# Kernel tuning notes

Hardware: AMD Instinct MI355X
Metric: run time of the kernel (lower is better)

The kernel has to match this reference:

```python
import jax, jax.numpy as jnp
import numpy as np

B, IN, OUT = 8192, 4096, 4096


def setup_inputs() -> dict:
    key = jax.random.key(0)
    k_x, k_qw, k_qb, k_pw, k_pb, k_eps, k_ps = jax.random.split(key, 7)
    x = jax.random.normal(k_x, (B, IN), jnp.float32)
    # Posterior / prior means: weight (OUT, IN) and bias (OUT,), fused as (OUT, IN+1)
    q_w = 0.05 * jax.random.normal(k_qw, (OUT, IN), jnp.float32)
    q_b = 0.05 * jax.random.normal(k_qb, (OUT,), jnp.float32)
    p_w = 0.05 * jax.random.normal(k_pw, (OUT, IN), jnp.float32)
    p_b = 0.05 * jax.random.normal(k_pb, (OUT,), jnp.float32)
    q_mu = jnp.concatenate([q_w, q_b[:, None]], axis=1)  # (OUT, IN+1)
    p_mu = jnp.concatenate([p_w, p_b[:, None]], axis=1)  # (OUT, IN+1)
    # Matches torch init: cat(0.5*log|w|, 0.5*log|b|) == 0.5*log|cat(w, b)|
    q_log_sigma = 0.5 * jnp.log(jnp.abs(q_mu))
    # Explicit reparameterization noise (torch.randn_like made deterministic)
    eps = jax.random.normal(k_eps, (OUT, IN + 1), jnp.float32)
    p_log_sigma = jnp.asarray(-2.0, jnp.float32)  # scalar prior log-std
    return {"x": x, "p_log_sigma": p_log_sigma, "q_mu": q_mu,
            "q_log_sigma": q_log_sigma, "p_mu": p_mu, "eps": eps}


def reference(x, p_log_sigma, q_mu, q_log_sigma, p_mu, eps):
    # Append ones column to absorb the bias (torch.cat([x, ones], dim=1))
    x_aug = jnp.concatenate([x, jnp.ones((x.shape[0], 1), x.dtype)], axis=1)  # (B, IN+1)
    q_sigma = jnp.exp(q_log_sigma)
    p_sigma = jnp.exp(p_log_sigma)
    # Reparameterized weight sample
    weights = q_mu + q_sigma * eps  # (OUT, IN+1)
    # KL(N(p_mu, p_sigma) || N(q_mu, q_sigma)) summed elementwise (diag branch)
    kl = jnp.sum(p_log_sigma - q_log_sigma
                 + (q_sigma ** 2 + (p_mu - q_mu) ** 2) / (2.0 * p_sigma ** 2)
                 - 0.5)
    # F.linear(x_aug, weights, zeros(OUT))
    outputs = x_aug @ weights.T  # (B, OUT)
    return outputs, kl
```

## Files before the change

### kernel.cpp

```cpp
#include <hip/hip_runtime.h>
#include <cstdint>
#include <cstddef>

#define K_PAD 4128
#define BKg 32
#define NT 129

typedef __bf16 bf16x8 __attribute__((ext_vector_type(8)));
typedef float f32x4 __attribute__((ext_vector_type(4)));

__device__ __forceinline__ unsigned short f2bf(float f) {
  unsigned int u = __float_as_uint(f);
  u = (u + 0x7fffu + ((u >> 16) & 1u)) >> 16;
  return (unsigned short)u;
}

__device__ __forceinline__ void gload_lds16(const void* g, void* l) {
  __builtin_amdgcn_global_load_lds((const __attribute__((address_space(1))) void*)g,
                                   (__attribute__((address_space(3))) void*)l,
                                   16, 0, 0);
}

__global__ void k_xaug(const float* __restrict__ x, unsigned short* __restrict__ xa) {
  const int row = blockIdx.x;
  const int t = threadIdx.x;
  const float4* xr = (const float4*)(x + (size_t)row * 4096);
  unsigned short* out = xa + (size_t)row * K_PAD;
#pragma unroll
  for (int i = 0; i < 4; ++i) {
    const int g = t + i * 256;
    float4 v = xr[g];
    ushort4 o;
    o.x = f2bf(v.x); o.y = f2bf(v.y); o.z = f2bf(v.z); o.w = f2bf(v.w);
    *(ushort4*)(out + g * 4) = o;
  }
  if (t < 32) out[4096 + t] = (t == 0) ? (unsigned short)0x3F80 : (unsigned short)0;
}

__global__ void k_wkl(const float* __restrict__ q_mu, const float* __restrict__ q_ls,
                      const float* __restrict__ p_mu, const float* __restrict__ eps,
                      const float* __restrict__ p_ls, unsigned short* __restrict__ w,
                      float* __restrict__ kl_out) {
  const int row = blockIdx.x;
  const int t = threadIdx.x;
  const float pls = p_ls[0];
  const float inv2ps2 = 0.5f * __expf(-2.0f * pls);
  const size_t base = (size_t)row * 4097;
  unsigned short* wr = w + (size_t)row * K_PAD;
  float kl = 0.f;
  const float4* qm4 = (const float4*)(q_mu + base);
  const float4* ql4 = (const float4*)(q_ls + base);
  const float4* pm4 = (const float4*)(p_mu + base);
  const float4* ep4 = (const float4*)(eps + base);
  if ((((size_t)row * 4097) & 3) == 0) {
#pragma unroll 1
    for (int i = 0; i < 4; ++i) {
      const int g = t + i * 256;
      float4 qm = qm4[g], ql = ql4[g], pm = pm4[g], ep = ep4[g];
      float kls = 0.f;
      ushort4 o;
      {
        float qs = __expf(ql.x); float d = pm.x - qm.x;
        kls += (pls - ql.x) - 0.5f + (qs * qs + d * d) * inv2ps2;
        o.x = f2bf(__fmaf_rn(qs, ep.x, qm.x));
      }
      {
        float qs = __expf(ql.y); float d = pm.y - qm.y;
        kls += (pls - ql.y) - 0.5f + (qs * qs + d * d) * inv2ps2;
        o.y = f2bf(__fmaf_rn(qs, ep.y, qm.y));
      }
      {
        float qs = __expf(ql.z); float d = pm.z - qm.z;
        kls += (pls - ql.z) - 0.5f + (qs * qs + d * d) * inv2ps2;
        o.z = f2bf(__fmaf_rn(qs, ep.z, qm.z));
      }
      {
        float qs = __expf(ql.w); float d = pm.w - qm.w;
        kls += (pls - ql.w) - 0.5f + (qs * qs + d * d) * inv2ps2;
        o.w = f2bf(__fmaf_rn(qs, ep.w, qm.w));
      }
      kl += kls;
      *(ushort4*)(wr + g * 4) = o;
    }
    if (t == 0) {
      const int c = 4096;
      float qm = q_mu[base + c], ql = q_ls[base + c];
      float qs = __expf(ql);
      float d = p_mu[base + c] - qm;
      kl += (pls - ql) - 0.5f + (qs * qs + d * d) * inv2ps2;
      wr[c] = f2bf(__fmaf_rn(qs, eps[base + c], qm));
    }
    if (t < 31) wr[4097 + t] = 0;
  } else {
#pragma unroll 1
    for (int i = 0; i < 17; ++i) {
      const int c = t + i * 256;
      if (c < 4097) {
        float qm = q_mu[base + c];
        float ql = q_ls[base + c];
        float qs = __expf(ql);
        float e  = eps[base + c];
        float pm = p_mu[base + c];
        float d = pm - qm;
        kl += (pls - ql) - 0.5f + (qs * qs + d * d) * inv2ps2;
        wr[c] = f2bf(__fmaf_rn(qs, e, qm));
      } else if (c < K_PAD) {
        wr[c] = 0;
      }
    }
  }
#pragma unroll
  for (int off = 32; off > 0; off >>= 1) kl += __shfl_down(kl, off, 64);
  __shared__ float part[4];
  const int wave = t >> 6, lane = t & 63;
  if (lane == 0) part[wave] = kl;
  __syncthreads();
  if (t == 0) atomicAdd(kl_out, part[0] + part[1] + part[2] + part[3]);
}

__global__ __launch_bounds__(512, 2) void k_gemm(const unsigned short* __restrict__ A,
                                                 const unsigned short* __restrict__ Bm,
                                                 float* __restrict__ C) {
  __shared__ unsigned short As[3][256 * 32];
  __shared__ unsigned short Bs[3][256 * 32];
  const int t = threadIdx.x;
  const int wave = t >> 6;
  const int lane = t & 63;
  const int wm = wave >> 2;
  const int wn = wave & 3;
  const int rowBase = blockIdx.y * 256;
  const int colBase = blockIdx.x * 256;
  const int fr = lane & 15;
  const int kg = lane >> 4;

  f32x4 acc[8][4] = {};

  const unsigned short* Abase = A + (size_t)rowBase * K_PAD;
  const unsigned short* Bbase = Bm + (size_t)colBase * K_PAD;

  const int rs = t >> 2;
  const int kc = ((t & 3) ^ ((t >> 3) & 3)) * 8;
  const int lds0 = (wave * 64) * 8;
  const int lds1 = (512 + wave * 64) * 8;

  int aOff[8], bOff[4];
#pragma unroll
  for (int i = 0; i < 8; ++i) {
    const int ra = wm * 128 + i * 16 + fr;
    aOff[i] = (ra * 4 + (kg ^ ((ra >> 1) & 3))) * 8;
  }
#pragma unroll
  for (int j = 0; j < 4; ++j) {
    const int rbr = wn * 64 + j * 16 + fr;
    bOff[j] = (rbr * 4 + (kg ^ ((rbr >> 1) & 3))) * 8;
  }

#define STAGE(SB, K0)                                                              \
  do {                                                                             \
    gload_lds16(Abase + (size_t)rs * K_PAD + (K0) + kc, &As[SB][lds0]);            \
    gload_lds16(Abase + (size_t)(rs + 128) * K_PAD + (K0) + kc, &As[SB][lds1]);    \
    gload_lds16(Bbase + (size_t)rs * K_PAD + (K0) + kc, &Bs[SB][lds0]);            \
    gload_lds16(Bbase + (size_t)(rs + 128) * K_PAD + (K0) + kc, &Bs[SB][lds1]);    \
  } while (0)

  STAGE(0, 0);
  STAGE(1, BKg);
  asm volatile("s_waitcnt vmcnt(4)" ::: "memory");
  __builtin_amdgcn_s_barrier();
  asm volatile("" ::: "memory");

#define BODY(RB, SB, KT)                                                           \
  do {                                                                             \
    int kn = (KT) + 2; if (kn > NT - 1) kn = NT - 1;    \
    STAGE(SB, kn * BKg);                                                           \
    bf16x8 af[4], bfv[4];                                                          \
    _Pragma("unroll") for (int j = 0; j < 4; ++j)                                  \
      bfv[j] = *(const bf16x8*)&Bs[RB][bOff[j]];                                   \
    _Pragma("unroll") for (int i = 0; i < 4; ++i)                                  \
      af[i] = *(const bf16x8*)&As[RB][aOff[i]];                                    \
    __builtin_amdgcn_s_setprio(1);                                                 \
    _Pragma("unroll") for (int i = 0; i < 4; ++i)                                  \
      _Pragma("unroll") for (int j = 0; j < 4; ++j)                                \
        acc[i][j] = __builtin_amdgcn_mfma_f32_16x16x32_bf16(af[i], bfv[j],         \
                                                            acc[i][j], 0, 0, 0);  \
    __builtin_amdgcn_s_setprio(0);                                                 \
    _Pragma("unroll") for (int i = 0; i < 4; ++i)                                  \
      af[i] = *(const bf16x8*)&As[RB][aOff[4 + i]];                                \
    __builtin_amdgcn_s_setprio(1);                                                 \
    _Pragma("unroll") for (int i = 0; i < 4; ++i)                                  \
      _Pragma("unroll") for (int j = 0; j < 4; ++j)                                \
        acc[4 + i][j] = __builtin_amdgcn_mfma_f32_16x16x32_bf16(af[i], bfv[j],     \
                                                                acc[4 + i][j],    \
                                                                0, 0, 0);          \
    __builtin_amdgcn_s_setprio(0);                                                 \
    asm volatile("s_waitcnt vmcnt(4)" ::: "memory");       \
    __builtin_amdgcn_s_barrier();                                                  \
    asm volatile("" ::: "memory");                                                 \
  } while (0)

#pragma unroll 1
  for (int kt = 0; kt < NT; kt += 3) {
    BODY(0, 2, kt);
    BODY(1, 0, kt + 1);
    BODY(2, 1, kt + 2);
  }

#undef BODY
#undef STAGE

  const int cr = (lane >> 4) * 4;
  const int cc = lane & 15;
#pragma unroll
  for (int i = 0; i < 8; ++i) {
#pragma unroll
    for (int j = 0; j < 4; ++j) {
      const int col = colBase + wn * 64 + j * 16 + cc;
#pragma unroll
      for (int r = 0; r < 4; ++r) {
        const int row = rowBase + wm * 128 + i * 16 + cr + r;
        C[(size_t)row * 4096 + col] = acc[i][j][r];
      }
    }
  }
}

extern "C" void kernel_launch(void* const* d_in, const int* in_sizes, int n_in,
                              void* d_out, int out_size, void* d_ws, size_t ws_size,
                              hipStream_t stream) {
  const float* x      = (const float*)d_in[0];
  const float* p_ls   = (const float*)d_in[1];
  const float* q_mu   = (const float*)d_in[2];
  const float* q_lsig = (const float*)d_in[3];
  const float* p_mu   = (const float*)d_in[4];
  const float* eps    = (const float*)d_in[5];
  float* out = (float*)d_out;
  float* kl_out = out + (size_t)8192 * 4096;

  unsigned short* xa   = (unsigned short*)d_ws;
  unsigned short* wmat = xa + (size_t)8192 * K_PAD;

  hipMemsetAsync(kl_out, 0, sizeof(float), stream);
  k_xaug<<<8192, 256, 0, stream>>>(x, xa);
  k_wkl<<<4096, 256, 0, stream>>>(q_mu, q_lsig, p_mu, eps, p_ls, wmat, kl_out);
  k_gemm<<<dim3(16, 32), 512, 0, stream>>>(xa, wmat, out);
}
```

Before: 707.9 us.

## Restructure GEMM to BK=64 double-buffered phased pipeline and flatten weight-sample kernel

The GEMM main loop moves from a triple-buffered 32-wide K tile to a double-buffered 64-wide K tile. It uses an XOR swizzle over 8 chunks and explicit ds_read_b128 asm with fixed offsets. Each tile is split into four MFMA quadrants, with LDS reads and global-to-LDS stage issues interleaved between barriers, to overlap loads with compute and cut barrier count per K. The weight/KL kernel now walks the flat (OUT, IN+1) buffer with aligned float4 loads for every block and maps indices back to padded rows with a magic-number divide, which removes the unaligned scalar path. K padding grows to 4160, so both GEMM operands carry a little more zero data. The extra barriers per tile and the scalar 2-byte scattered stores may limit the gain.

```diff
diff --git a/kernel.cpp b/kernel.cpp
--- a/kernel.cpp
+++ b/kernel.cpp
@@ -2,9 +2,8 @@
 #include <cstdint>
 #include <cstddef>
 
-#define K_PAD 4128
-#define BKg 32
-#define NT 129
+#define K_PAD 4160
+#define NT 65
 
 typedef __bf16 bf16x8 __attribute__((ext_vector_type(8)));
 typedef float f32x4 __attribute__((ext_vector_type(4)));
@@ -34,79 +33,54 @@
     o.x = f2bf(v.x); o.y = f2bf(v.y); o.z = f2bf(v.z); o.w = f2bf(v.w);
     *(ushort4*)(out + g * 4) = o;
   }
-  if (t < 32) out[4096 + t] = (t == 0) ? (unsigned short)0x3F80 : (unsigned short)0;
+  if (t < 64) out[4096 + t] = (t == 0) ? (unsigned short)0x3F80 : (unsigned short)0;
 }
 
 __global__ void k_wkl(const float* __restrict__ q_mu, const float* __restrict__ q_ls,
                       const float* __restrict__ p_mu, const float* __restrict__ eps,
                       const float* __restrict__ p_ls, unsigned short* __restrict__ w,
                       float* __restrict__ kl_out) {
-  const int row = blockIdx.x;
+  const int b = blockIdx.x;
   const int t = threadIdx.x;
   const float pls = p_ls[0];
   const float inv2ps2 = 0.5f * __expf(-2.0f * pls);
-  const size_t base = (size_t)row * 4097;
-  unsigned short* wr = w + (size_t)row * K_PAD;
   float kl = 0.f;
-  const float4* qm4 = (const float4*)(q_mu + base);
-  const float4* ql4 = (const float4*)(q_ls + base);
-  const float4* pm4 = (const float4*)(p_mu + base);
-  const float4* ep4 = (const float4*)(eps + base);
-  if ((((size_t)row * 4097) & 3) == 0) {
+  if (b < 4096 && t < 63) w[(size_t)b * K_PAD + 4097 + t] = 0;
 #pragma unroll 1
-    for (int i = 0; i < 4; ++i) {
-      const int g = t + i * 256;
-      float4 qm = qm4[g], ql = ql4[g], pm = pm4[g], ep = ep4[g];
-      float kls = 0.f;
-      ushort4 o;
-      {
-        float qs = __expf(ql.x); float d = pm.x - qm.x;
-        kls += (pls - ql.x) - 0.5f + (qs * qs + d * d) * inv2ps2;
-        o.x = f2bf(__fmaf_rn(qs, ep.x, qm.x));
-      }
-      {
-        float qs = __expf(ql.y); float d = pm.y - qm.y;
-        kls += (pls - ql.y) - 0.5f + (qs * qs + d * d) * inv2ps2;
-        o.y = f2bf(__fmaf_rn(qs, ep.y, qm.y));
-      }
-      {
-        float qs = __expf(ql.z); float d = pm.z - qm.z;
-        kls += (pls - ql.z) - 0.5f + (qs * qs + d * d) * inv2ps2;
-        o.z = f2bf(__fmaf_rn(qs, ep.z, qm.z));
-      }
-      {
-        float qs = __expf(ql.w); float d = pm.w - qm.w;
-        kls += (pls - ql.w) - 0.5f + (qs * qs + d * d) * inv2ps2;
-        o.w = f2bf(__fmaf_rn(qs, ep.w, qm.w));
-      }
-      kl += kls;
-      *(ushort4*)(wr + g * 4) = o;
-    }
-    if (t == 0) {
-      const int c = 4096;
-      float qm = q_mu[base + c], ql = q_ls[base + c];
-      float qs = __expf(ql);
-      float d = p_mu[base + c] - qm;
-      kl += (pls - ql) - 0.5f + (qs * qs + d * d) * inv2ps2;
-      wr[c] = f2bf(__fmaf_rn(qs, eps[base + c], qm));
-    }
-    if (t < 31) wr[4097 + t] = 0;
-  } else {
-#pragma unroll 1
-    for (int i = 0; i < 17; ++i) {
-      const int c = t + i * 256;
-      if (c < 4097) {
-        float qm = q_mu[base + c];
-        float ql = q_ls[base + c];
-        float qs = __expf(ql);
-        float e  = eps[base + c];
-        float pm = p_mu[base + c];
-        float d = pm - qm;
-        kl += (pls - ql) - 0.5f + (qs * qs + d * d) * inv2ps2;
-        wr[c] = f2bf(__fmaf_rn(qs, e, qm));
-      } else if (c < K_PAD) {
-        wr[c] = 0;
-      }
+  for (int i = 0; i < 4; ++i) {
+    const unsigned g = (unsigned)b * 1024u + (unsigned)i * 256u + (unsigned)t;
+    const unsigned f = g * 4u;
+    const float4 qm = *(const float4*)(q_mu + f);
+    const float4 ql = *(const float4*)(q_ls + f);
+    const float4 pm = *(const float4*)(p_mu + f);
+    const float4 ep = *(const float4*)(eps + f);
+    unsigned short o[4];
+    {
+      float qs = __expf(ql.x); float d = pm.x - qm.x;
+      kl += (pls - ql.x) - 0.5f + (qs * qs + d * d) * inv2ps2;
+      o[0] = f2bf(__fmaf_rn(qs, ep.x, qm.x));
+    }
+    {
+      float qs = __expf(ql.y); float d = pm.y - qm.y;
+      kl += (pls - ql.y) - 0.5f + (qs * qs + d * d) * inv2ps2;
+      o[1] = f2bf(__fmaf_rn(qs, ep.y, qm.y));
+    }
+    {
+      float qs = __expf(ql.z); float d = pm.z - qm.z;
+      kl += (pls - ql.z) - 0.5f + (qs * qs + d * d) * inv2ps2;
+      o[2] = f2bf(__fmaf_rn(qs, ep.z, qm.z));
+    }
+    {
+      float qs = __expf(ql.w); float d = pm.w - qm.w;
+      kl += (pls - ql.w) - 0.5f + (qs * qs + d * d) * inv2ps2;
+      o[3] = f2bf(__fmaf_rn(qs, ep.w, qm.w));
+    }
+    unsigned row = (unsigned)(((unsigned long long)f * 33546242ull) >> 37);
+    unsigned col = f - row * 4097u;
+#pragma unroll
+    for (int e = 0; e < 4; ++e) {
+      w[(size_t)row * K_PAD + col] = o[e];
+      if (++col == 4097u) { col = 0; ++row; }
     }
   }
 #pragma unroll
@@ -121,8 +95,8 @@
 __global__ __launch_bounds__(512, 2) void k_gemm(const unsigned short* __restrict__ A,
                                                  const unsigned short* __restrict__ Bm,
                                                  float* __restrict__ C) {
-  __shared__ unsigned short As[3][256 * 32];
-  __shared__ unsigned short Bs[3][256 * 32];
+  __shared__ unsigned short As[2][256 * 64];
+  __shared__ unsigned short Bs[2][256 * 64];
   const int t = threadIdx.x;
   const int wave = t >> 6;
   const int lane = t & 63;
@@ -134,79 +108,110 @@
   const int kg = lane >> 4;
 
   f32x4 acc[8][4] = {};
-
-  const unsigned short* Abase = A + (size_t)rowBase * K_PAD;
-  const unsigned short* Bbase = Bm + (size_t)colBase * K_PAD;
-
-  const int rs = t >> 2;
-  const int kc = ((t & 3) ^ ((t >> 3) & 3)) * 8;
-  const int lds0 = (wave * 64) * 8;
-  const int lds1 = (512 + wave * 64) * 8;
-
-  int aOff[8], bOff[4];
-#pragma unroll
-  for (int i = 0; i < 8; ++i) {
-    const int ra = wm * 128 + i * 16 + fr;
-    aOff[i] = (ra * 4 + (kg ^ ((ra >> 1) & 3))) * 8;
-  }
-#pragma unroll
-  for (int j = 0; j < 4; ++j) {
-    const int rbr = wn * 64 + j * 16 + fr;
-    bOff[j] = (rbr * 4 + (kg ^ ((rbr >> 1) & 3))) * 8;
-  }
-
-#define STAGE(SB, K0)                                                              \
-  do {                                                                             \
-    gload_lds16(Abase + (size_t)rs * K_PAD + (K0) + kc, &As[SB][lds0]);            \
-    gload_lds16(Abase + (size_t)(rs + 128) * K_PAD + (K0) + kc, &As[SB][lds1]);    \
-    gload_lds16(Bbase + (size_t)rs * K_PAD + (K0) + kc, &Bs[SB][lds0]);            \
-    gload_lds16(Bbase + (size_t)(rs + 128) * K_PAD + (K0) + kc, &Bs[SB][lds1]);    \
-  } while (0)
-
-  STAGE(0, 0);
-  STAGE(1, BKg);
-  asm volatile("s_waitcnt vmcnt(4)" ::: "memory");
-  __builtin_amdgcn_s_barrier();
-  asm volatile("" ::: "memory");
-
-#define BODY(RB, SB, KT)                                                           \
-  do {                                                                             \
-    int kn = (KT) + 2; if (kn > NT - 1) kn = NT - 1;    \
-    STAGE(SB, kn * BKg);                                                           \
-    bf16x8 af[4], bfv[4];                                                          \
-    _Pragma("unroll") for (int j = 0; j < 4; ++j)                                  \
-      bfv[j] = *(const bf16x8*)&Bs[RB][bOff[j]];                                   \
-    _Pragma("unroll") for (int i = 0; i < 4; ++i)                                  \
-      af[i] = *(const bf16x8*)&As[RB][aOff[i]];                                    \
-    __builtin_amdgcn_s_setprio(1);                                                 \
-    _Pragma("unroll") for (int i = 0; i < 4; ++i)                                  \
-      _Pragma("unroll") for (int j = 0; j < 4; ++j)                                \
-        acc[i][j] = __builtin_amdgcn_mfma_f32_16x16x32_bf16(af[i], bfv[j],         \
-                                                            acc[i][j], 0, 0, 0);  \
-    __builtin_amdgcn_s_setprio(0);                                                 \
-    _Pragma("unroll") for (int i = 0; i < 4; ++i)                                  \
-      af[i] = *(const bf16x8*)&As[RB][aOff[4 + i]];                                \
-    __builtin_amdgcn_s_setprio(1);                                                 \
-    _Pragma("unroll") for (int i = 0; i < 4; ++i)                                  \
-      _Pragma("unroll") for (int j = 0; j < 4; ++j)                                \
-        acc[4 + i][j] = __builtin_amdgcn_mfma_f32_16x16x32_bf16(af[i], bfv[j],     \
-                                                                acc[4 + i][j],    \
-                                                                0, 0, 0);          \
-    __builtin_amdgcn_s_setprio(0);                                                 \
-    asm volatile("s_waitcnt vmcnt(4)" ::: "memory");       \
-    __builtin_amdgcn_s_barrier();                                                  \
-    asm volatile("" ::: "memory");                                                 \
-  } while (0)
+  bf16x8 aA[2][4];
+  bf16x8 bF[2][4];
+
+  const unsigned colx0 = (((unsigned)kg) ^ ((unsigned)fr & 7u)) * 16u;
+  const unsigned colx1 = (((unsigned)kg + 4u) ^ ((unsigned)fr & 7u)) * 16u;
+  const unsigned aLds = (unsigned)(uintptr_t)&As[0][0];
+  const unsigned bLds = (unsigned)(uintptr_t)&Bs[0][0];
+  const unsigned aAddr0 = aLds + (unsigned)(wm * 128 + fr) * 128u + colx0;
+  const unsigned aAddr1 = aLds + (unsigned)(wm * 128 + fr) * 128u + colx1;
+  const unsigned bAddr0 = bLds + (unsigned)(wn * 64 + fr) * 128u + colx0;
+  const unsigned bAddr1 = bLds + (unsigned)(wn * 64 + fr) * 128u + colx1;
+
+  const unsigned gcol8 = (((unsigned)t & 7u) ^ (((unsigned)t >> 3) & 7u)) * 8u;
+  const unsigned short* Asrc = A + (size_t)(rowBase + (t >> 3)) * K_PAD + gcol8;
+  const unsigned short* Bsrc = Bm + (size_t)(colBase + (t >> 3)) * K_PAD + gcol8;
+
+#define DSR_O(dst, addr, OFS) \
+  asm volatile("ds_read_b128 %0, %1 offset:" OFS : "=v"(dst) : "v"(addr))
+#define BAR __builtin_amdgcn_s_barrier()
+#define LGKM0                                             \
+  do {                                                    \
+    asm volatile("s_waitcnt lgkmcnt(0)" ::: "memory");    \
+    __builtin_amdgcn_sched_barrier(0);                    \
+  } while (0)
+#define VM8 asm volatile("s_waitcnt vmcnt(8)" ::: "memory")
+
+#define STAGE(DST, S, SRC, KB)                                                  \
+  do {                                                                          \
+    gload_lds16((SRC) + (KB),                 &DST[S][0 * 4096 + wave * 512]);  \
+    gload_lds16((SRC) + (KB) + 64 * K_PAD,    &DST[S][1 * 4096 + wave * 512]);  \
+    gload_lds16((SRC) + (KB) + 128 * K_PAD,   &DST[S][2 * 4096 + wave * 512]);  \
+    gload_lds16((SRC) + (KB) + 192 * K_PAD,   &DST[S][3 * 4096 + wave * 512]);  \
+  } while (0)
+
+#define MMQ(IB, JB)                                                             \
+  do {                                                                          \
+    _Pragma("unroll") for (int i_ = 0; i_ < 4; ++i_) {                          \
+      _Pragma("unroll") for (int j_ = 0; j_ < 2; ++j_) {                        \
+        acc[(IB) + i_][(JB) + j_] = __builtin_amdgcn_mfma_f32_16x16x32_bf16(    \
+            aA[0][i_], bF[0][(JB) + j_], acc[(IB) + i_][(JB) + j_], 0, 0, 0);   \
+        acc[(IB) + i_][(JB) + j_] = __builtin_amdgcn_mfma_f32_16x16x32_bf16(    \
+            aA[1][i_], bF[1][(JB) + j_], acc[(IB) + i_][(JB) + j_], 0, 0, 0);   \
+      }                                                                         \
+    }                                                                           \
+  } while (0)
+
+#define TILE(S, T)                                                              \
+  do {                                                                          \
+    const int kn_ = ((T) + 2 > NT - 1) ? (NT - 1) : ((T) + 2);                  \
+    const size_t kb_ = (size_t)kn_ * 64;                                        \
+    const unsigned aS0 = aAddr0 + (S) * 32768u, aS1 = aAddr1 + (S) * 32768u;    \
+    const unsigned bS0 = bAddr0 + (S) * 32768u, bS1 = bAddr1 + (S) * 32768u;    \
+                                \
+    DSR_O(aA[0][0], aS0, "0");    DSR_O(aA[0][1], aS0, "2048");                 \
+    DSR_O(aA[0][2], aS0, "4096"); DSR_O(aA[0][3], aS0, "6144");                 \
+    DSR_O(aA[1][0], aS1, "0");    DSR_O(aA[1][1], aS1, "2048");                 \
+    DSR_O(aA[1][2], aS1, "4096"); DSR_O(aA[1][3], aS1, "6144");                 \
+    DSR_O(bF[0][0], bS0, "0");    DSR_O(bF[0][1], bS0, "2048");                 \
+    DSR_O(bF[1][0], bS1, "0");    DSR_O(bF[1][1], bS1, "2048");                 \
+    BAR; LGKM0;                                                                 \
+    __builtin_amdgcn_s_setprio(1); MMQ(0, 0); __builtin_amdgcn_s_setprio(0);    \
+    BAR;                                                                        \
+                                                        \
+    DSR_O(bF[0][2], bS0, "4096"); DSR_O(bF[0][3], bS0, "6144");                 \
+    DSR_O(bF[1][2], bS1, "4096"); DSR_O(bF[1][3], bS1, "6144");                 \
+    BAR; LGKM0;                                                                 \
+    __builtin_amdgcn_s_setprio(1); MMQ(0, 2); __builtin_amdgcn_s_setprio(0);    \
+    BAR;                                                                        \
+           \
+    DSR_O(aA[0][0], aS0, "8192");  DSR_O(aA[0][1], aS0, "10240");               \
+    DSR_O(aA[0][2], aS0, "12288"); DSR_O(aA[0][3], aS0, "14336");               \
+    DSR_O(aA[1][0], aS1, "8192");  DSR_O(aA[1][1], aS1, "10240");               \
+    DSR_O(aA[1][2], aS1, "12288"); DSR_O(aA[1][3], aS1, "14336");               \
+    STAGE(Bs, S, Bsrc, kb_);                                                    \
+    BAR; LGKM0;                                                                 \
+    __builtin_amdgcn_s_setprio(1); MMQ(4, 0); __builtin_amdgcn_s_setprio(0);    \
+    BAR;                                                                        \
+                \
+    STAGE(As, S, Asrc, kb_);                                                    \
+    BAR;                                                                        \
+    __builtin_amdgcn_s_setprio(1); MMQ(4, 2); __builtin_amdgcn_s_setprio(0);    \
+    VM8; BAR;                                                                   \
+  } while (0)
+
+  STAGE(Bs, 0, Bsrc, 0);
+  STAGE(As, 0, Asrc, 0);
+  STAGE(Bs, 1, Bsrc, 64);
+  STAGE(As, 1, Asrc, 64);
+  VM8; BAR;
 
 #pragma unroll 1
-  for (int kt = 0; kt < NT; kt += 3) {
-    BODY(0, 2, kt);
-    BODY(1, 0, kt + 1);
-    BODY(2, 1, kt + 2);
-  }
-
-#undef BODY
+  for (int tp = 0; tp < 32; ++tp) {
+    TILE(0, 2 * tp);
+    TILE(1, 2 * tp + 1);
+  }
+  TILE(0, 64);
+
+#undef TILE
+#undef MMQ
 #undef STAGE
+#undef VM8
+#undef LGKM0
+#undef BAR
+#undef DSR_O
 
   const int cr = (lane >> 4) * 4;
   const int cc = lane & 15;
@@ -241,6 +246,6 @@
 
   hipMemsetAsync(kl_out, 0, sizeof(float), stream);
   k_xaug<<<8192, 256, 0, stream>>>(x, xa);
-  k_wkl<<<4096, 256, 0, stream>>>(q_mu, q_lsig, p_mu, eps, p_ls, wmat, kl_out);
+  k_wkl<<<4097, 256, 0, stream>>>(q_mu, q_lsig, p_mu, eps, p_ls, wmat, kl_out);
   k_gemm<<<dim3(16, 32), 512, 0, stream>>>(xa, wmat, out);
 }
```

New measurement: 628.3 us. 1.13x faster.
